# Kernel tuning notes

Hardware: AMD Instinct MI355X
Metric: run time of the kernel (lower is better)

The kernel has to match this reference:

```python
import jax, jax.numpy as jnp
import numpy as np

MODES = 32
NUM_BLOCKS = 4
NUM_EXPERTS = 16
TOP_K = 4
TEMPERATURE = 2.0


def _gelu(t):
    return jax.nn.gelu(t, approximate=False)  # torch F.gelu default (erf)


def _c1(x, w, b):
    # 1x1 conv: x [B,C,H,W], w [O,C], b [O]
    return jnp.einsum('bchw,oc->bohw', x, w) + b[None, :, None, None]


def _group_norm(x, w, b, groups=8, eps=1e-5):
    B, C, H, W = x.shape
    xg = x.reshape(B, groups, C // groups, H, W)
    mu = xg.mean(axis=(2, 3, 4), keepdims=True)
    var = xg.var(axis=(2, 3, 4), keepdims=True)
    xn = ((xg - mu) * jax.lax.rsqrt(var + eps)).reshape(B, C, H, W)
    return xn * w[None, :, None, None] + b[None, :, None, None]


def _bn_eval(x, g, b, rm, rv, eps=1e-5):
    # eval-mode BatchNorm with running stats
    return (x - rm) * jax.lax.rsqrt(rv + eps) * g + b


def _afno(x, w1, b1, w2, b2):
    # x: [B,C,H,W] (channel_first). Block-diagonal complex MLP on low FFT modes.
    B, C, H, W = x.shape
    bs = C // NUM_BLOCKS
    xp = x.transpose(0, 2, 3, 1)                      # [B,H,W,C]
    xf = jnp.fft.rfft2(xp, axes=(1, 2), norm='ortho') # [B,H,Wf,C] complex64
    Wf = xf.shape[2]
    xf = xf.reshape(B, H, Wf, NUM_BLOCKS, bs)
    m = MODES
    xm = xf[:, :m, :m]                                # kept modes only
    xr, xi = xm.real, xm.imag
    o1r = _gelu(jnp.einsum('bhwni,nio->bhwno', xr, w1[0])
                - jnp.einsum('bhwni,nio->bhwno', xi, w1[1]) + b1[0])
    o1i = _gelu(jnp.einsum('bhwni,nio->bhwno', xi, w1[0])
                + jnp.einsum('bhwni,nio->bhwno', xr, w1[1]) + b1[1])
    o2r = (jnp.einsum('bhwni,nio->bhwno', o1r, w2[0])
           - jnp.einsum('bhwni,nio->bhwno', o1i, w2[1]) + b2[0])
    o2i = (jnp.einsum('bhwni,nio->bhwno', o1i, w2[0])
           + jnp.einsum('bhwni,nio->bhwno', o1r, w2[1]) + b2[1])
    of = jnp.zeros((B, H, Wf, NUM_BLOCKS, bs), dtype=xf.dtype)
    of = of.at[:, :m, :m].set(o2r + 1j * o2i)
    out = jnp.fft.irfft2(of.reshape(B, H, Wf, C), s=(H, W), axes=(1, 2), norm='ortho')
    out = out + xp
    return out.transpose(0, 3, 1, 2)


def _forward(x, gn1_w, gn1_b, afno_w1, afno_b1, afno_w2, afno_b2,
             gn2_w, gn2_b, fe_w, fe_b, g1_w, g1_b, bn1_g, bn1_b, bn1_rm, bn1_rv,
             ca_w1, ca_b1, ca_w2, ca_b2, g2_w, g2_b, bn2_g, bn2_b, bn2_rm, bn2_rv,
             g3_w, g3_b, shared_w, shared_b, expert_w, expert_b):
    residual = x
    h = _group_norm(x, gn1_w, gn1_b)
    h = _afno(h, afno_w1, afno_b1, afno_w2, afno_b2)
    h = h + residual            # double_skip
    residual = h
    h = _group_norm(h, gn2_w, gn2_b)
    # MoEImage (eval mode -> loss_gate = 0)
    feats = _gelu(_c1(h, fe_w, fe_b))
    shared = jnp.zeros_like(h)
    for s in range(shared_w.shape[0]):
        shared = shared + _gelu(_c1(feats, shared_w[s], shared_b[s])) / shared_w.shape[0]
    # gating on global-avg-pooled features (1x1 convs == linears)
    gf = feats.mean(axis=(2, 3))                              # [B,C]
    h1 = _gelu(_bn_eval(gf @ g1_w.T + g1_b, bn1_g, bn1_b, bn1_rm, bn1_rv))
    a = _gelu(h1 @ ca_w1.T + ca_b1) @ ca_w2.T + ca_b2
    h1 = h1 * jax.nn.sigmoid(2.0 * a)                          # avg==max pool on 1x1 map
    h2 = _gelu(_bn_eval(h1 @ g2_w.T + g2_b, bn2_g, bn2_b, bn2_rm, bn2_rv))
    scores = h2 @ g3_w.T + g3_b                                # [B,E]
    vals, idx = jax.lax.top_k(scores, TOP_K)
    wts = jax.nn.softmax(vals / TEMPERATURE, axis=1)
    B = x.shape[0]
    gate_w = jnp.zeros((B, NUM_EXPERTS), x.dtype).at[jnp.arange(B)[:, None], idx].add(wts)
    out = shared
    for e in range(NUM_EXPERTS):
        out = out + _gelu(_c1(feats, expert_w[e], expert_b[e])) * gate_w[:, e][:, None, None, None]
    return out + residual


def setup_inputs():
    key = jax.random.key(0)
    ks = jax.random.split(key, 16)
    B, C, H, W = 8, 64, 192, 192
    nb = NUM_BLOCKS
    bs = C // nb
    E = NUM_EXPERTS
    scale = 1.0 / (bs * bs)
    f32 = jnp.float32
    n = lambda k, shape: jax.random.normal(k, shape, f32) * 0.02
    return {
        'x': jax.random.normal(ks[0], (B, C, H, W), f32),
        'gn1_w': jnp.ones((C,), f32), 'gn1_b': jnp.zeros((C,), f32),
        'afno_w1': jax.random.uniform(ks[1], (2, nb, bs, bs), f32) * scale,
        'afno_b1': jax.random.uniform(ks[2], (2, nb, bs), f32) * scale,
        'afno_w2': jax.random.uniform(ks[3], (2, nb, bs, bs), f32) * scale,
        'afno_b2': jax.random.uniform(ks[4], (2, nb, bs), f32) * scale,
        'gn2_w': jnp.ones((C,), f32), 'gn2_b': jnp.zeros((C,), f32),
        'fe_w': n(ks[5], (C, C)), 'fe_b': jnp.zeros((C,), f32),
        'g1_w': n(ks[6], (2 * C, C)), 'g1_b': jnp.zeros((2 * C,), f32),
        'bn1_g': jnp.ones((2 * C,), f32), 'bn1_b': jnp.zeros((2 * C,), f32),
        'bn1_rm': jnp.zeros((2 * C,), f32), 'bn1_rv': jnp.ones((2 * C,), f32),
        'ca_w1': n(ks[7], (2 * C // 16, 2 * C)), 'ca_b1': jnp.zeros((2 * C // 16,), f32),
        'ca_w2': n(ks[8], (2 * C, 2 * C // 16)), 'ca_b2': jnp.zeros((2 * C,), f32),
        'g2_w': n(ks[9], (C, 2 * C)), 'g2_b': jnp.zeros((C,), f32),
        'bn2_g': jnp.ones((C,), f32), 'bn2_b': jnp.zeros((C,), f32),
        'bn2_rm': jnp.zeros((C,), f32), 'bn2_rv': jnp.ones((C,), f32),
        'g3_w': n(ks[10], (E, C)), 'g3_b': jnp.zeros((E,), f32),
        'shared_w': n(ks[11], (2, C, C)), 'shared_b': jnp.zeros((2, C), f32),
        'expert_w': n(ks[12], (E, C, C)), 'expert_b': jnp.zeros((E, C), f32),
    }


def reference(x, gn1_w, gn1_b, afno_w1, afno_b1, afno_w2, afno_b2,
              gn2_w, gn2_b, fe_w, fe_b, g1_w, g1_b, bn1_g, bn1_b, bn1_rm, bn1_rv,
              ca_w1, ca_b1, ca_w2, ca_b2, g2_w, g2_b, bn2_g, bn2_b, bn2_rm, bn2_rv,
              g3_w, g3_b, shared_w, shared_b, expert_w, expert_b):
    return _forward(x, gn1_w, gn1_b, afno_w1, afno_b1, afno_w2, afno_b2,
                    gn2_w, gn2_b, fe_w, fe_b, g1_w, g1_b, bn1_g, bn1_b, bn1_rm, bn1_rv,
                    ca_w1, ca_b1, ca_w2, ca_b2, g2_w, g2_b, bn2_g, bn2_b, bn2_rm, bn2_rv,
                    g3_w, g3_b, shared_w, shared_b, expert_w, expert_b)
```

## Files before the change

### kernel.cpp

```cpp
#include <hip/hip_runtime.h>
#include <math.h>

#define TPI 6.283185307179586f

typedef __attribute__((ext_vector_type(8))) short bf8v;
typedef __attribute__((ext_vector_type(4))) float f4v;

#define MFMA(a,b,c) __builtin_amdgcn_mfma_f32_16x16x32_bf16((a),(b),(c),0,0,0)

__device__ __forceinline__ float gelu_f(float v){
  return 0.5f*v*(1.0f+erff(v*0.7071067811865475f));
}
__device__ __forceinline__ float gelu_fast(float x){
  float x2=x*x;
  float inner=fmaf(0.044715f*x2, x, x);
  float e=__expf(1.5957691216057308f*inner);
  float r=__builtin_amdgcn_rcpf(1.0f+e);
  return fmaf(-x, r, x);
}
__device__ __forceinline__ float gelu_sig(float x){
  float e=__expf(-1.702f*x);
  return x*__builtin_amdgcn_rcpf(1.0f+e);
}
__device__ __forceinline__ unsigned short f2b(float f){
  union{float f; unsigned u;} v; v.f=f;
  unsigned r=v.u + 0x7FFFu + ((v.u>>16)&1u);
  return (unsigned short)(r>>16);
}

__global__ __launch_bounds__(256) void prep(const float* __restrict__ shw, const float* __restrict__ exw,
    const float* __restrict__ shb, const float* __restrict__ exb, const float* __restrict__ few,
    unsigned short* __restrict__ T, unsigned short* __restrict__ wall, float* __restrict__ ball,
    unsigned short* __restrict__ wfe, float* __restrict__ gfp){
  const float a = TPI/192.0f;
  int stride=gridDim.x*256;
  for(int i=blockIdx.x*256+threadIdx.x; i<61440; i+=stride){
    float v;
    if(i<12288){
      int n1=i/192, w=i%192; int kw=n1>>1, c=n1&1;
      int m=(kw*w)%192; float cs,sn; sincosf((float)m*a,&sn,&cs);
      v = c ? -sn : cs;
    } else if(i<36864){
      int j=i-12288; int n1=j/384, k1=j%384; int kh=n1>>1, d=n1&1; int h=k1>>1, c=k1&1;
      int m=(kh*h)%192; float cs,sn; sincosf((float)m*a,&sn,&cs);
      float e = d ? (c ? cs : -sn) : (c ? sn : cs);
      v = e*(1.0f/192.0f);
    } else if(i<49152){
      int j=i-36864; int h=j/64, k1=j%64; int kh=k1>>1, c=k1&1;
      int m=(h*kh)%192; float cs,sn; sincosf((float)m*a,&sn,&cs);
      v = c ? sn : cs;
    } else {
      int j=i-49152; int w=j/64, k1=j%64; int kw=k1>>1, d=k1&1;
      float f = kw ? (2.0f/192.0f) : (1.0f/192.0f);
      int m=(w*kw)%192; float cs,sn; sincosf((float)m*a,&sn,&cs);
      v = d ? -f*sn : f*cs;
    }
    T[i]=f2b(v);
  }
  for(int i=blockIdx.x*256+threadIdx.x;i<73728;i+=stride) wall[i]=f2b(i<8192?shw[i]:exw[i-8192]);
  for(int i=blockIdx.x*256+threadIdx.x;i<1152;i+=stride)  ball[i]=(i<128)?shb[i]:exb[i-128];
  for(int i=blockIdx.x*256+threadIdx.x;i<4096;i+=stride)  wfe[i]=f2b(few[i]);
  for(int i=blockIdx.x*256+threadIdx.x;i<512;i+=stride)   gfp[i]=0.f;
}

__global__ void gn_finalize(const float* __restrict__ part, const float* __restrict__ gw,
                            const float* __restrict__ gb, float2* __restrict__ sb){
  int g=threadIdx.x; if(g>=64) return;
  float S=0,SS=0;
  for(int j=0;j<8;j++){ S+=part[(g*8+j)*2]; SS+=part[(g*8+j)*2+1]; }
  const float inv=1.0f/294912.0f;
  float mean=S*inv, var=SS*inv-mean*mean;
  float rstd=rsqrtf(var+1e-5f);
  int b=g>>3, gg=g&7;
  for(int k=0;k<8;k++){
    int c=gg*8+k;
    float sc=rstd*gw[c];
    sb[b*64+c]=make_float2(sc, gb[c]-mean*sc);
  }
}

__global__ __launch_bounds__(256) void fwd_dft(const float* __restrict__ x,
      const unsigned short* __restrict__ TBf1, const unsigned short* __restrict__ TBf2,
      float* __restrict__ Xm2, float* __restrict__ part1){
  __shared__ __align__(16) unsigned short ldsA[64*200];
  __shared__ __align__(16) float sX[2048];
  __shared__ float red[8];
  int t=threadIdx.x, bc=blockIdx.x;
  int wave=t>>6, l=t&63, lr=l&15, lg=l>>4;
  const float* xch = x + (size_t)bc*36864;
  for(int i=t;i<1536;i+=256){
    int row=i/24, chunk=i%24;
    *(uint4*)&ldsA[row*200 + chunk*8] = *(const uint4*)(TBf1 + row*192 + chunk*8);
  }
  __syncthreads();
  float s_=0.f, ss_=0.f;
  f4v acc1[3][4];
  for(int mt=0;mt<3;mt++){
    int m0=(wave+mt*4)*16;
    const float* xrow = xch + (m0+lr)*192 + lg*8;
    bf8v af[6];
    #pragma unroll
    for(int ks=0;ks<6;ks++){
      float4 u0=*(const float4*)(xrow+ks*32);
      float4 u1=*(const float4*)(xrow+ks*32+4);
      s_ += u0.x+u0.y+u0.z+u0.w+u1.x+u1.y+u1.z+u1.w;
      ss_+= u0.x*u0.x+u0.y*u0.y+u0.z*u0.z+u0.w*u0.w
           +u1.x*u1.x+u1.y*u1.y+u1.z*u1.z+u1.w*u1.w;
      bf8v a;
      a[0]=(short)f2b(u0.x); a[1]=(short)f2b(u0.y); a[2]=(short)f2b(u0.z); a[3]=(short)f2b(u0.w);
      a[4]=(short)f2b(u1.x); a[5]=(short)f2b(u1.y); a[6]=(short)f2b(u1.z); a[7]=(short)f2b(u1.w);
      af[ks]=a;
    }
    #pragma unroll
    for(int nt=0;nt<4;nt++){
      f4v acc={0.f,0.f,0.f,0.f};
      #pragma unroll
      for(int ks=0;ks<6;ks++){
        bf8v b=*(const bf8v*)&ldsA[(nt*16+lr)*200 + ks*32 + lg*8];
        acc=MFMA(af[ks],b,acc);
      }
      acc1[mt][nt]=acc;
    }
  }
  __syncthreads();
  for(int mt=0;mt<3;mt++){
    int m0=(wave+mt*4)*16;
    #pragma unroll
    for(int nt=0;nt<4;nt++){
      int n1=nt*16+lr; int kw=n1>>1, c=n1&1;
      #pragma unroll
      for(int reg=0;reg<4;reg++){
        int h=m0+4*lg+reg;
        ldsA[kw*392 + 2*h + c]=f2b(acc1[mt][nt][reg]);
      }
    }
  }
  __syncthreads();
  for(int pp=0;pp<2;pp++){
    int p=wave+pp*4;
    int m0=(p>>2)*16, n0=(p&3)*16;
    f4v acc={0.f,0.f,0.f,0.f};
    #pragma unroll
    for(int ks=0;ks<12;ks++){
      bf8v a=*(const bf8v*)&ldsA[(m0+lr)*392 + ks*32 + lg*8];
      bf8v b=*(const bf8v*)(TBf2 + (n0+lr)*384 + ks*32 + lg*8);
      acc=MFMA(a,b,acc);
    }
    int n1=n0+lr; int kh=n1>>1, d=n1&1;
    #pragma unroll
    for(int reg=0;reg<4;reg++){
      int kw=m0+4*lg+reg;
      sX[(kh*32+kw)*2 + d]=acc[reg];
    }
  }
  __syncthreads();
  float* dst=Xm2+(size_t)bc*2048;
  for(int i=t;i<512;i+=256) *(float4*)(dst+i*4)=*(const float4*)(sX+i*4);
  #pragma unroll
  for(int o=32;o>0;o>>=1){ s_+=__shfl_down(s_,o); ss_+=__shfl_down(ss_,o); }
  if(l==0){ red[wave]=s_; red[4+wave]=ss_; }
  __syncthreads();
  if(t==0){
    part1[bc*2]  =red[0]+red[1]+red[2]+red[3];
    part1[bc*2+1]=red[4]+red[5]+red[6]+red[7];
  }
}

__global__ __launch_bounds__(256) void mode_mlp(const float* __restrict__ Xm2, const float2* __restrict__ sb1,
    const float* __restrict__ w1, const float* __restrict__ b1,
    const float* __restrict__ w2, const float* __restrict__ b2,
    float* __restrict__ S2){
  __shared__ float w10[1024], w11[1024], w20[1024], w21[1024];
  __shared__ float b10[64], b11[64], b20[64], b21[64];
  __shared__ float2 sbl[64];
  __shared__ float xr[32][64], xi[32][64];
  __shared__ float o1r[32][64], o1i[32][64];
  int t=threadIdx.x;
  int b=blockIdx.x>>5, kh=blockIdx.x&31;
  for(int i=t;i<1024;i+=256){ w10[i]=w1[i]; w11[i]=w1[1024+i]; w20[i]=w2[i]; w21[i]=w2[1024+i]; }
  if(t<64){ b10[t]=b1[t]; b11[t]=b1[64+t]; b20[t]=b2[t]; b21[t]=b2[64+t]; sbl[t]=sb1[b*64+t]; }
  __syncthreads();
  for(int q=0;q<16;q++){
    int idx=q*256+t; int c=idx>>6, jj=idx&63;
    float2 s=sbl[c];
    float v=Xm2[((size_t)(b*64+c))*2048 + kh*64 + jj]*s.x;
    if(kh==0 && jj==0) v += 192.0f*s.y;
    if(jj&1) xi[jj>>1][c]=v; else xr[jj>>1][c]=v;
  }
  __syncthreads();
  int tl=t&63, n=tl>>4, o=tl&15, wb=n*256+o;
  #pragma unroll
  for(int it=0;it<8;it++){
    int kw=(t>>6)+it*4;
    float a_r=b10[tl], a_i=b11[tl];
    #pragma unroll
    for(int i=0;i<16;i++){
      float rr=xr[kw][n*16+i], im=xi[kw][n*16+i];
      float W0=w10[wb+i*16], W1=w11[wb+i*16];
      a_r=fmaf(rr,W0,fmaf(-im,W1,a_r));
      a_i=fmaf(im,W0,fmaf( rr,W1,a_i));
    }
    o1r[kw][tl]=gelu_f(a_r); o1i[kw][tl]=gelu_f(a_i);
  }
  __syncthreads();
  #pragma unroll
  for(int it=0;it<8;it++){
    int kw=(t>>6)+it*4;
    float c_r=b20[tl], c_i=b21[tl];
    #pragma unroll
    for(int i=0;i<16;i++){
      float rr=o1r[kw][n*16+i], im=o1i[kw][n*16+i];
      float W0=w20[wb+i*16], W1=w21[wb+i*16];
      c_r=fmaf(rr,W0,fmaf(-im,W1,c_r));
      c_i=fmaf(im,W0,fmaf( rr,W1,c_i));
    }
    xr[kw][tl]=c_r; xi[kw][tl]=c_i;
  }
  __syncthreads();
  for(int q=0;q<16;q++){
    int idx=q*256+t; int c=idx>>6, jj=idx&63;
    float v = (jj&1) ? xi[jj>>1][c] : xr[jj>>1][c];
    S2[((size_t)(b*64+c))*2048 + kh*64 + jj]=v;
  }
}

__global__ __launch_bounds__(256) void inv_dft(const float* __restrict__ S2,
      const unsigned short* __restrict__ TAi, const unsigned short* __restrict__ TBi,
      const float* __restrict__ x, const float2* __restrict__ sb,
      float* __restrict__ h2, float* __restrict__ part2){
  __shared__ __align__(16) unsigned short Bs[64*72];
  __shared__ __align__(16) unsigned short GL[192*72];
  __shared__ float red[8];
  int t=threadIdx.x, bc=blockIdx.x;
  int wave=t>>6, l=t&63, lr=l&15, lg=l>>4;
  const float* sp=S2+(size_t)bc*2048;
  for(int i=t;i<1024;i+=256){
    int kh=i>>5, kw=i&31;
    float Sr=sp[(kh*32+kw)*2], Si=sp[(kh*32+kw)*2+1];
    unsigned short br=f2b(Sr), bi_=f2b(Si), nbi=f2b(-Si);
    Bs[(2*kw+0)*72 + 2*kh+0]=br;
    Bs[(2*kw+0)*72 + 2*kh+1]=nbi;
    Bs[(2*kw+1)*72 + 2*kh+0]=bi_;
    Bs[(2*kw+1)*72 + 2*kh+1]=br;
  }
  __syncthreads();
  for(int mt=0;mt<3;mt++){
    int m0=(wave+mt*4)*16;
    bf8v a0=*(const bf8v*)(TAi + (m0+lr)*64 + lg*8);
    bf8v a1=*(const bf8v*)(TAi + (m0+lr)*64 + 32 + lg*8);
    #pragma unroll
    for(int nt=0;nt<4;nt++){
      f4v acc={0.f,0.f,0.f,0.f};
      bf8v b0=*(const bf8v*)&Bs[(nt*16+lr)*72 + lg*8];
      bf8v b1=*(const bf8v*)&Bs[(nt*16+lr)*72 + 32 + lg*8];
      acc=MFMA(a0,b0,acc); acc=MFMA(a1,b1,acc);
      #pragma unroll
      for(int reg=0;reg<4;reg++)
        GL[(m0+4*lg+reg)*72 + nt*16+lr]=f2b(acc[reg]);
    }
  }
  __syncthreads();
  float2 sv=sb[bc];
  float cA=sv.x+1.0f, cB=sv.y;
  asm volatile("" : "+v"(cA), "+v"(cB));
  const float* xch=x+(size_t)bc*36864;
  float* och=h2+(size_t)bc*36864;
  float s_=0.f, ss_=0.f;
  for(int mt=0;mt<3;mt++){
    int m0=(wave+mt*4)*16;
    bf8v a0=*(const bf8v*)&GL[(m0+lr)*72 + lg*8];
    bf8v a1=*(const bf8v*)&GL[(m0+lr)*72 + 32 + lg*8];
    for(int nt=0;nt<12;nt++){
      int n0=nt*16;
      f4v acc={0.f,0.f,0.f,0.f};
      bf8v b0=*(const bf8v*)(TBi + (n0+lr)*64 + lg*8);
      bf8v b1=*(const bf8v*)(TBi + (n0+lr)*64 + 32 + lg*8);
      acc=MFMA(a0,b0,acc); acc=MFMA(a1,b1,acc);
      int w=n0+lr;
      #pragma unroll
      for(int reg=0;reg<4;reg++){
        int h=m0+4*lg+reg;
        int ga=h*192+w;
        float xv=xch[ga];
        float val=acc[reg]+fmaf(cA,xv,cB);
        och[ga]=val;
        s_+=val; ss_+=val*val;
      }
    }
  }
  #pragma unroll
  for(int o=32;o>0;o>>=1){ s_+=__shfl_down(s_,o); ss_+=__shfl_down(ss_,o); }
  if(l==0){ red[wave]=s_; red[4+wave]=ss_; }
  __syncthreads();
  if(t==0){
    part2[bc*2]  =red[0]+red[1]+red[2]+red[3];
    part2[bc*2+1]=red[4]+red[5]+red[6]+red[7];
  }
}

__global__ __launch_bounds__(256,4) void gf_k(const float* __restrict__ h2, const float2* __restrict__ sb,
    const unsigned short* __restrict__ wfe, const float* __restrict__ feb,
    float* __restrict__ gfp){
  __shared__ __align__(16) unsigned short A[128*72];
  __shared__ float sgf[64];
  int t=threadIdx.x;
  int blk=blockIdx.x, b=blk/288, tile=blk-b*288, hw0=tile*128;
  if(t<64) sgf[t]=0.f;
  for(int i=t;i<2048;i+=256){
    int c=i>>5, q=i&31;
    float2 s=sb[b*64+c];
    float4 v=*(const float4*)&h2[(size_t)(b*64+c)*36864 + hw0 + q*4];
    int px0=q*4, sw=((px0>>4)&3)<<3, cc=c^sw;
    A[(px0+0)*72+cc]=f2b(fmaf(v.x,s.x,s.y));
    A[(px0+1)*72+cc]=f2b(fmaf(v.y,s.x,s.y));
    A[(px0+2)*72+cc]=f2b(fmaf(v.z,s.x,s.y));
    A[(px0+3)*72+cc]=f2b(fmaf(v.w,s.x,s.y));
  }
  __syncthreads();
  int wave=t>>6, l=t&63, lr=l&15, lg=l>>4;
  int pxb=wave*32;
  bf8v af[2][2];
  #pragma unroll
  for(int fm=0;fm<2;fm++){
    int row=pxb+fm*16+lr, sw=((row>>4)&3)<<3;
    #pragma unroll
    for(int ks=0;ks<2;ks++) af[fm][ks]=*(const bf8v*)&A[row*72+((ks*32+lg*8)^sw)];
  }
  float gsum[4]={0.f,0.f,0.f,0.f};
  #pragma unroll
  for(int fn=0;fn<4;fn++){
    bf8v b0=*(const bf8v*)(wfe+(fn*16+lr)*64+lg*8);
    bf8v b1=*(const bf8v*)(wfe+(fn*16+lr)*64+32+lg*8);
    float bs=feb[fn*16+lr];
    #pragma unroll
    for(int fm=0;fm<2;fm++){
      f4v acc={0.f,0.f,0.f,0.f};
      acc=MFMA(af[fm][0],b0,acc);
      acc=MFMA(af[fm][1],b1,acc);
      #pragma unroll
      for(int r=0;r<4;r++) gsum[fn]+=gelu_fast(acc[r]+bs);
    }
  }
  #pragma unroll
  for(int fn=0;fn<4;fn++){
    float v=gsum[fn];
    v+=__shfl_xor(v,16); v+=__shfl_xor(v,32);
    if(lg==0) atomicAdd(&sgf[fn*16+lr], v);
  }
  __syncthreads();
  if(t<64) atomicAdd(&gfp[b*64+t], sgf[t]);
}

__global__ __launch_bounds__(128) void gating(const float* __restrict__ gfp,
  const float* __restrict__ g1w, const float* __restrict__ g1b,
  const float* __restrict__ bn1g, const float* __restrict__ bn1b, const float* __restrict__ bn1m, const float* __restrict__ bn1v,
  const float* __restrict__ cw1, const float* __restrict__ cb1, const float* __restrict__ cw2, const float* __restrict__ cb2,
  const float* __restrict__ g2w, const float* __restrict__ g2b,
  const float* __restrict__ bn2g, const float* __restrict__ bn2b, const float* __restrict__ bn2m, const float* __restrict__ bn2v,
  const float* __restrict__ g3w, const float* __restrict__ g3b, float2* __restrict__ act){
  __shared__ float gf[8][64];
  __shared__ float h1[8][128];
  __shared__ float a1[8][8];
  __shared__ float h2g[8][64];
  __shared__ float sc[8][16];
  int t=threadIdx.x;
  for(int i=t;i<512;i+=128) gf[i>>6][i&63]=gfp[i]*(1.0f/36864.0f);
  __syncthreads();
  for(int i=t;i<1024;i+=128){
    int b=i>>7, j=i&127;
    float s=g1b[j];
    for(int c=0;c<64;c++) s=fmaf(gf[b][c], g1w[j*64+c], s);
    s=(s-bn1m[j])*rsqrtf(bn1v[j]+1e-5f)*bn1g[j]+bn1b[j];
    h1[b][j]=gelu_f(s);
  }
  __syncthreads();
  if(t<64){
    int b=t>>3, k=t&7; float s=cb1[k];
    for(int j=0;j<128;j++) s=fmaf(h1[b][j], cw1[k*128+j], s);
    a1[b][k]=gelu_f(s);
  }
  __syncthreads();
  for(int i=t;i<1024;i+=128){
    int b=i>>7, j=i&127;
    float s=cb2[j];
    for(int k=0;k<8;k++) s=fmaf(a1[b][k], cw2[j*8+k], s);
    h1[b][j]=h1[b][j]/(1.0f+expf(-2.0f*s));
  }
  __syncthreads();
  for(int i=t;i<512;i+=128){
    int b=i>>6, j=i&63;
    float s=g2b[j];
    for(int k=0;k<128;k++) s=fmaf(h1[b][k], g2w[j*128+k], s);
    s=(s-bn2m[j])*rsqrtf(bn2v[j]+1e-5f)*bn2g[j]+bn2b[j];
    h2g[b][j]=gelu_f(s);
  }
  __syncthreads();
  {
    int b=t>>4, e=t&15;
    float s=g3b[e];
    for(int c=0;c<64;c++) s=fmaf(h2g[b][c], g3w[e*64+c], s);
    sc[b][e]=s;
  }
  __syncthreads();
  if(t<8){
    int b=t;
    float v[16];
    for(int e=0;e<16;e++) v[e]=sc[b][e];
    float vals[4]; int idx[4];
    for(int k=0;k<4;k++){
      float best=-1e30f; int bi=0;
      for(int e=0;e<16;e++) if(v[e]>best){best=v[e];bi=e;}
      vals[k]=best; idx[k]=bi; v[bi]=-1e30f;
    }
    float m=vals[0], ssum=0.f, w[4];
    for(int k=0;k<4;k++){ w[k]=expf((vals[k]-m)*0.5f); ssum+=w[k]; }
    act[b*6+0]=make_float2(0.5f, __int_as_float(0));
    act[b*6+1]=make_float2(0.5f, __int_as_float(1));
    for(int k=0;k<4;k++) act[b*6+2+k]=make_float2(w[k]/ssum, __int_as_float(2+idx[k]));
  }
}

__global__ __launch_bounds__(256,4) void final_k(const float* __restrict__ h2, const float2* __restrict__ sb,
  const unsigned short* __restrict__ wfe, const float* __restrict__ feb,
  const unsigned short* __restrict__ wall, const float* __restrict__ ball,
  const float2* __restrict__ act, float* __restrict__ out){
  __shared__ __align__(16) unsigned short A[128*72];
  int t=threadIdx.x;
  int blk=blockIdx.x, b=blk/288, tile=blk-b*288, hw0=tile*128;
  for(int i=t;i<2048;i+=256){
    int c=i>>5, q=i&31;
    float2 s=sb[b*64+c];
    float4 v=*(const float4*)&h2[(size_t)(b*64+c)*36864 + hw0 + q*4];
    int px0=q*4, sw=((px0>>4)&3)<<3, cc=c^sw;
    A[(px0+0)*72+cc]=f2b(fmaf(v.x,s.x,s.y));
    A[(px0+1)*72+cc]=f2b(fmaf(v.y,s.x,s.y));
    A[(px0+2)*72+cc]=f2b(fmaf(v.z,s.x,s.y));
    A[(px0+3)*72+cc]=f2b(fmaf(v.w,s.x,s.y));
  }
  __syncthreads();
  int wave=t>>6, l=t&63, lr=l&15, lg=l>>4;
  int pxb=wave*32;
  {
    bf8v af[2][2];
    #pragma unroll
    for(int fm=0;fm<2;fm++){
      int row=pxb+fm*16+lr, sw=((row>>4)&3)<<3;
      #pragma unroll
      for(int ks=0;ks<2;ks++) af[fm][ks]=*(const bf8v*)&A[row*72+((ks*32+lg*8)^sw)];
    }
    #pragma unroll
    for(int fn=0;fn<4;fn++){
      bf8v b0=*(const bf8v*)(wfe+(fn*16+lr)*64+lg*8);
      bf8v b1=*(const bf8v*)(wfe+(fn*16+lr)*64+32+lg*8);
      float bs=feb[fn*16+lr];
      #pragma unroll
      for(int fm=0;fm<2;fm++){
        f4v acc={0.f,0.f,0.f,0.f};
        acc=MFMA(af[fm][0],b0,acc);
        acc=MFMA(af[fm][1],b1,acc);
        int swm=(((pxb+fm*16)>>4)&3)<<3;
        int cc=(fn*16+lr)^swm;
        #pragma unroll
        for(int r=0;r<4;r++)
          A[(pxb+fm*16+4*lg+r)*72+cc]=f2b(gelu_fast(acc[r]+bs));
      }
    }
  }
  bf8v af2[2][2];
  #pragma unroll
  for(int fm=0;fm<2;fm++){
    int row=pxb+fm*16+lr, sw=((row>>4)&3)<<3;
    #pragma unroll
    for(int ks=0;ks<2;ks++) af2[fm][ks]=*(const bf8v*)&A[row*72+((ks*32+lg*8)^sw)];
  }
  float* Fo=(float*)A;
  #pragma unroll
  for(int half=0;half<2;half++){
    float oa[2][2][4]={};
    for(int j=0;j<6;j++){
      float2 aw=act[b*6+j];
      int term=__float_as_int(aw.y);
      float g=aw.x;
      const unsigned short* wp=wall+term*4096;
      const float* bp=ball+term*64;
      #pragma unroll
      for(int fn2=0;fn2<2;fn2++){
        int fn=half*2+fn2;
        bf8v b0=*(const bf8v*)(wp+(fn*16+lr)*64+lg*8);
        bf8v b1=*(const bf8v*)(wp+(fn*16+lr)*64+32+lg*8);
        float bs=bp[fn*16+lr];
        #pragma unroll
        for(int fm=0;fm<2;fm++){
          f4v acc={0.f,0.f,0.f,0.f};
          acc=MFMA(af2[fm][0],b0,acc);
          acc=MFMA(af2[fm][1],b1,acc);
          #pragma unroll
          for(int r=0;r<4;r++)
            oa[fm][fn2][r]=fmaf(g, gelu_sig(acc[r]+bs), oa[fm][fn2][r]);
        }
      }
    }
    __syncthreads();
    #pragma unroll
    for(int fm=0;fm<2;fm++)
      #pragma unroll
      for(int fn2=0;fn2<2;fn2++){
        int ocl=fn2*16+lr;
        *(float4*)&Fo[ocl*132 + pxb + fm*16 + 4*lg] =
            make_float4(oa[fm][fn2][0],oa[fm][fn2][1],oa[fm][fn2][2],oa[fm][fn2][3]);
      }
    __syncthreads();
    for(int i=t;i<1024;i+=256){
      int ocl=i>>5, px0=(i&31)*4;
      int oc=half*32+ocl;
      size_t base=(size_t)(b*64+oc)*36864 + hw0 + px0;
      float4 rv=*(const float4*)&out[base];
      float4 ov=*(const float4*)&Fo[ocl*132+px0];
      *(float4*)&out[base]=make_float4(ov.x+rv.x,ov.y+rv.y,ov.z+rv.z,ov.w+rv.w);
    }
  }
}

extern "C" void kernel_launch(void* const* d_in, const int* in_sizes, int n_in,
                              void* d_out, int out_size, void* d_ws, size_t ws_size,
                              hipStream_t stream){
  const float* x    =(const float*)d_in[0];
  const float* gn1w =(const float*)d_in[1];
  const float* gn1b =(const float*)d_in[2];
  const float* aw1  =(const float*)d_in[3];
  const float* ab1  =(const float*)d_in[4];
  const float* aw2  =(const float*)d_in[5];
  const float* ab2  =(const float*)d_in[6];
  const float* gn2w =(const float*)d_in[7];
  const float* gn2b =(const float*)d_in[8];
  const float* few  =(const float*)d_in[9];
  const float* feb  =(const float*)d_in[10];
  const float* g1w  =(const float*)d_in[11];
  const float* g1b  =(const float*)d_in[12];
  const float* bn1g =(const float*)d_in[13];
  const float* bn1b =(const float*)d_in[14];
  const float* bn1m =(const float*)d_in[15];
  const float* bn1v =(const float*)d_in[16];
  const float* cw1  =(const float*)d_in[17];
  const float* cb1  =(const float*)d_in[18];
  const float* cw2  =(const float*)d_in[19];
  const float* cb2  =(const float*)d_in[20];
  const float* g2w  =(const float*)d_in[21];
  const float* g2b  =(const float*)d_in[22];
  const float* bn2g =(const float*)d_in[23];
  const float* bn2b =(const float*)d_in[24];
  const float* bn2m =(const float*)d_in[25];
  const float* bn2v =(const float*)d_in[26];
  const float* g3w  =(const float*)d_in[27];
  const float* g3b  =(const float*)d_in[28];
  const float* shw  =(const float*)d_in[29];
  const float* shb  =(const float*)d_in[30];
  const float* exw  =(const float*)d_in[31];
  const float* exb  =(const float*)d_in[32];

  float* out=(float*)d_out;
  float* ws=(float*)d_ws;

  float*  part1 = ws;
  float*  part2 = ws+1024;
  float2* sb1   = (float2*)(ws+2048);
  float2* sb2   = (float2*)(ws+3072);
  float2* act   = (float2*)(ws+4096);
  float*  gfp   = ws+4224;
  float*  Xm2   = ws+8192;
  float*  S2    = ws+1056768;
  unsigned short* Tbl  = (unsigned short*)(ws+2105344);
  unsigned short* wall = (unsigned short*)(ws+2136064);
  float*          ball = ws+2172928;
  unsigned short* wfe  = (unsigned short*)(ws+2174080);
  const unsigned short* TBf1 = Tbl;
  const unsigned short* TBf2 = Tbl+12288;
  const unsigned short* TAi  = Tbl+36864;
  const unsigned short* TBi  = Tbl+49152;

  prep<<<64,256,0,stream>>>(shw, exw, shb, exb, few, Tbl, wall, ball, wfe, gfp);
  fwd_dft <<<512,256,0,stream>>>(x, TBf1, TBf2, Xm2, part1);
  gn_finalize<<<1,64,0,stream>>>(part1, gn1w, gn1b, sb1);
  mode_mlp<<<256,256,0,stream>>>(Xm2, sb1, aw1, ab1, aw2, ab2, S2);
  inv_dft <<<512,256,0,stream>>>(S2, TAi, TBi, x, sb1, out, part2);
  gn_finalize<<<1,64,0,stream>>>(part2, gn2w, gn2b, sb2);
  gf_k<<<2304,256,0,stream>>>(out, sb2, wfe, feb, gfp);
  gating <<<1,128,0,stream>>>(gfp, g1w,g1b, bn1g,bn1b,bn1m,bn1v,
                              cw1,cb1,cw2,cb2, g2w,g2b, bn2g,bn2b,bn2m,bn2v,
                              g3w,g3b, act);
  final_k<<<2304,256,0,stream>>>(out, sb2, wfe, feb, wall, ball, act, out);
}
```

Measured before the change: 223.9 us.

## Cache bf16 fe-conv GELU features from gating pass for reuse in final kernel

```diff
diff --git a/kernel.cpp b/kernel.cpp
--- a/kernel.cpp
+++ b/kernel.cpp
@@ -300,21 +300,27 @@
 
 __global__ __launch_bounds__(256,4) void gf_k(const float* __restrict__ h2, const float2* __restrict__ sb,
     const unsigned short* __restrict__ wfe, const float* __restrict__ feb,
-    float* __restrict__ gfp){
+    float* __restrict__ gfp, unsigned short* __restrict__ feats){
   __shared__ __align__(16) unsigned short A[128*72];
   __shared__ float sgf[64];
   int t=threadIdx.x;
   int blk=blockIdx.x, b=blk/288, tile=blk-b*288, hw0=tile*128;
   if(t<64) sgf[t]=0.f;
-  for(int i=t;i<2048;i+=256){
-    int c=i>>5, q=i&31;
+  float4 v[8];
+  #pragma unroll
+  for(int k=0;k<8;k++){
+    int i=t+k*256; int c=i>>5, q=i&31;
+    v[k]=*(const float4*)&h2[(size_t)(b*64+c)*36864 + hw0 + q*4];
+  }
+  #pragma unroll
+  for(int k=0;k<8;k++){
+    int i=t+k*256; int c=i>>5, q=i&31;
     float2 s=sb[b*64+c];
-    float4 v=*(const float4*)&h2[(size_t)(b*64+c)*36864 + hw0 + q*4];
     int px0=q*4, sw=((px0>>4)&3)<<3, cc=c^sw;
-    A[(px0+0)*72+cc]=f2b(fmaf(v.x,s.x,s.y));
-    A[(px0+1)*72+cc]=f2b(fmaf(v.y,s.x,s.y));
-    A[(px0+2)*72+cc]=f2b(fmaf(v.z,s.x,s.y));
-    A[(px0+3)*72+cc]=f2b(fmaf(v.w,s.x,s.y));
+    A[(px0+0)*72+cc]=f2b(fmaf(v[k].x,s.x,s.y));
+    A[(px0+1)*72+cc]=f2b(fmaf(v[k].y,s.x,s.y));
+    A[(px0+2)*72+cc]=f2b(fmaf(v[k].z,s.x,s.y));
+    A[(px0+3)*72+cc]=f2b(fmaf(v[k].w,s.x,s.y));
   }
   __syncthreads();
   int wave=t>>6, l=t&63, lr=l&15, lg=l>>4;
@@ -337,18 +343,29 @@
       f4v acc={0.f,0.f,0.f,0.f};
       acc=MFMA(af[fm][0],b0,acc);
       acc=MFMA(af[fm][1],b1,acc);
-      #pragma unroll
-      for(int r=0;r<4;r++) gsum[fn]+=gelu_fast(acc[r]+bs);
+      int swm=(((pxb+fm*16)>>4)&3)<<3;
+      int cc=(fn*16+lr)^swm;
+      #pragma unroll
+      for(int r=0;r<4;r++){
+        float g=gelu_fast(acc[r]+bs);
+        gsum[fn]+=g;
+        A[(pxb+fm*16+4*lg+r)*72+cc]=f2b(g);
+      }
     }
   }
   #pragma unroll
   for(int fn=0;fn<4;fn++){
-    float v=gsum[fn];
-    v+=__shfl_xor(v,16); v+=__shfl_xor(v,32);
-    if(lg==0) atomicAdd(&sgf[fn*16+lr], v);
+    float v2=gsum[fn];
+    v2+=__shfl_xor(v2,16); v2+=__shfl_xor(v2,32);
+    if(lg==0) atomicAdd(&sgf[fn*16+lr], v2);
   }
   __syncthreads();
   if(t<64) atomicAdd(&gfp[b*64+t], sgf[t]);
+  #pragma unroll
+  for(int k=0;k<4;k++){
+    int i=t+k*256; int px=i>>3, c0=(i&7)*8, sw=((px>>4)&3)<<3;
+    *(uint4*)&feats[(size_t)(b*36864+hw0+px)*64+c0] = *(const uint4*)&A[px*72+(c0^sw)];
+  }
 }
 
 __global__ __launch_bounds__(128) void gating(const float* __restrict__ gfp,
@@ -420,52 +437,26 @@
   }
 }
 
-__global__ __launch_bounds__(256,4) void final_k(const float* __restrict__ h2, const float2* __restrict__ sb,
-  const unsigned short* __restrict__ wfe, const float* __restrict__ feb,
+__global__ __launch_bounds__(256,4) void final_k(const unsigned short* __restrict__ feats,
   const unsigned short* __restrict__ wall, const float* __restrict__ ball,
   const float2* __restrict__ act, float* __restrict__ out){
   __shared__ __align__(16) unsigned short A[128*72];
   int t=threadIdx.x;
   int blk=blockIdx.x, b=blk/288, tile=blk-b*288, hw0=tile*128;
-  for(int i=t;i<2048;i+=256){
-    int c=i>>5, q=i&31;
-    float2 s=sb[b*64+c];
-    float4 v=*(const float4*)&h2[(size_t)(b*64+c)*36864 + hw0 + q*4];
-    int px0=q*4, sw=((px0>>4)&3)<<3, cc=c^sw;
-    A[(px0+0)*72+cc]=f2b(fmaf(v.x,s.x,s.y));
-    A[(px0+1)*72+cc]=f2b(fmaf(v.y,s.x,s.y));
-    A[(px0+2)*72+cc]=f2b(fmaf(v.z,s.x,s.y));
-    A[(px0+3)*72+cc]=f2b(fmaf(v.w,s.x,s.y));
+  uint4 fv[4];
+  #pragma unroll
+  for(int k=0;k<4;k++){
+    int i=t+k*256; int px=i>>3, c0=(i&7)*8;
+    fv[k]=*(const uint4*)&feats[(size_t)(b*36864+hw0+px)*64+c0];
+  }
+  #pragma unroll
+  for(int k=0;k<4;k++){
+    int i=t+k*256; int px=i>>3, c0=(i&7)*8, sw=((px>>4)&3)<<3;
+    *(uint4*)&A[px*72+(c0^sw)]=fv[k];
   }
   __syncthreads();
   int wave=t>>6, l=t&63, lr=l&15, lg=l>>4;
   int pxb=wave*32;
-  {
-    bf8v af[2][2];
-    #pragma unroll
-    for(int fm=0;fm<2;fm++){
-      int row=pxb+fm*16+lr, sw=((row>>4)&3)<<3;
-      #pragma unroll
-      for(int ks=0;ks<2;ks++) af[fm][ks]=*(const bf8v*)&A[row*72+((ks*32+lg*8)^sw)];
-    }
-    #pragma unroll
-    for(int fn=0;fn<4;fn++){
-      bf8v b0=*(const bf8v*)(wfe+(fn*16+lr)*64+lg*8);
-      bf8v b1=*(const bf8v*)(wfe+(fn*16+lr)*64+32+lg*8);
-      float bs=feb[fn*16+lr];
-      #pragma unroll
-      for(int fm=0;fm<2;fm++){
-        f4v acc={0.f,0.f,0.f,0.f};
-        acc=MFMA(af[fm][0],b0,acc);
-        acc=MFMA(af[fm][1],b1,acc);
-        int swm=(((pxb+fm*16)>>4)&3)<<3;
-        int cc=(fn*16+lr)^swm;
-        #pragma unroll
-        for(int r=0;r<4;r++)
-          A[(pxb+fm*16+4*lg+r)*72+cc]=f2b(gelu_fast(acc[r]+bs));
-      }
-    }
-  }
   bf8v af2[2][2];
   #pragma unroll
   for(int fm=0;fm<2;fm++){
@@ -573,6 +564,7 @@
   unsigned short* wall = (unsigned short*)(ws+2136064);
   float*          ball = ws+2172928;
   unsigned short* wfe  = (unsigned short*)(ws+2174080);
+  unsigned short* feats= (unsigned short*)(ws+2176128);
   const unsigned short* TBf1 = Tbl;
   const unsigned short* TBf2 = Tbl+12288;
   const unsigned short* TAi  = Tbl+36864;
@@ -584,9 +576,9 @@
   mode_mlp<<<256,256,0,stream>>>(Xm2, sb1, aw1, ab1, aw2, ab2, S2);
   inv_dft <<<512,256,0,stream>>>(S2, TAi, TBi, x, sb1, out, part2);
   gn_finalize<<<1,64,0,stream>>>(part2, gn2w, gn2b, sb2);
-  gf_k<<<2304,256,0,stream>>>(out, sb2, wfe, feb, gfp);
+  gf_k<<<2304,256,0,stream>>>(out, sb2, wfe, feb, gfp, feats);
   gating <<<1,128,0,stream>>>(gfp, g1w,g1b, bn1g,bn1b,bn1m,bn1v,
                               cw1,cb1,cw2,cb2, g2w,g2b, bn2g,bn2b,bn2m,bn2v,
                               g3w,g3b, act);
-  final_k<<<2304,256,0,stream>>>(out, sb2, wfe, feb, wall, ball, act, out);
-}
+  final_k<<<2304,256,0,stream>>>(feats, wall, ball, act, out);
+}
```

New measurement: 210.7 us. -5.9%, faster.
